# Optimization experiments

Measured on AMD Instinct MI355X. Metric: run time of the kernel, lower is better.

Reference implementation:

```python
import jax, jax.numpy as jnp
import numpy as np

H = 4096        # hidden_size
NH = 32         # heads
HD = H // NH    # head_dim = 128
EPS = 1e-5
MINUS_INF = -10000.0
B, S = 2, 1024


def setup_inputs() -> dict:
    key = jax.random.key(0)
    ks = jax.random.split(key, 7)
    x = jax.random.normal(ks[0], (B, S, H), jnp.float32)
    mask = jnp.zeros((B, 1, 1, S), jnp.float32)  # additive padding mask (0 = keep)
    norm_w = 1.0 + 0.02 * jax.random.normal(ks[1], (H,), jnp.float32)
    norm_b = 0.02 * jax.random.normal(ks[2], (H,), jnp.float32)
    qkv_w = 0.02 * jax.random.normal(ks[3], (H, 3 * H), jnp.float32)
    qkv_b = 0.02 * jax.random.normal(ks[4], (3 * H,), jnp.float32)
    attn_ow = 0.02 * jax.random.normal(ks[5], (H, H), jnp.float32)
    return {"x": x, "mask": mask, "norm_w": norm_w, "norm_b": norm_b,
            "qkv_w": qkv_w, "qkv_b": qkv_b, "attn_ow": attn_ow}


def reference(x, mask, norm_w, norm_b, qkv_w, qkv_b, attn_ow):
    b, s, h = x.shape
    # --- pre-attention layernorm (qkv_gemm fuses this in DeepSpeed) ---
    mu = jnp.mean(x, axis=-1, keepdims=True)
    var = jnp.mean(jnp.square(x - mu), axis=-1, keepdims=True)
    inp_norm = (x - mu) * jax.lax.rsqrt(var + EPS) * norm_w + norm_b
    # --- fused QKV GEMM + bias ---
    qkv = inp_norm @ qkv_w + qkv_b                      # [b, s, 3H]
    q, k, v = jnp.split(qkv, 3, axis=-1)
    q = q.reshape(b, s, NH, HD).transpose(0, 2, 1, 3)   # [b, nh, s, hd]
    k = k.reshape(b, s, NH, HD).transpose(0, 2, 1, 3)
    v = v.reshape(b, s, NH, HD).transpose(0, 2, 1, 3)
    # --- scaled dot-product with triangular (causal) mask + additive input mask ---
    norm_factor = 1.0 / jnp.sqrt(jnp.asarray(HD, x.dtype))
    scores = jnp.einsum('bhqd,bhkd->bhqk', q, k) * norm_factor  # [b, nh, s, s]
    causal = jnp.where(jnp.tril(jnp.ones((s, s), bool)), 0.0, MINUS_INF).astype(x.dtype)
    probs = jax.nn.softmax(scores + causal + mask, axis=-1)
    ctx = jnp.einsum('bhqk,bhkd->bhqd', probs, v)               # [b, nh, s, hd]
    ctx = ctx.transpose(0, 2, 1, 3).reshape(b, s, h)
    # --- output projection (vector_matmul, bias applied later in MLP residual-add) ---
    out = ctx @ attn_ow
    return out
```

## Files before the change

kernel.cpp:

```cpp
#include <hip/hip_runtime.h>
#include <stdint.h>


#define S_LEN 1024
#define HID   4096
#define NHEAD 32
#define HDIM  128

typedef __attribute__((ext_vector_type(8))) short bf16x8;
typedef __attribute__((ext_vector_type(4))) float f32x4;
typedef __attribute__((ext_vector_type(8))) unsigned short us8;

__device__ __forceinline__ unsigned short f2bf(float f) {
    union { float f; unsigned u; } v; v.f = f;
    unsigned r = v.u + 0x7fffu + ((v.u >> 16) & 1u);
    return (unsigned short)(r >> 16);
}

__device__ __forceinline__ void gld16(const unsigned short* g, unsigned short* l) {
    __builtin_amdgcn_global_load_lds(
        (const __attribute__((address_space(1))) void*)g,
        (__attribute__((address_space(3))) void*)l, 16, 0, 0);
}

__global__ __launch_bounds__(256) void ln_kernel(const float* __restrict__ x,
        const float* __restrict__ w, const float* __restrict__ bch,
        unsigned short* __restrict__ out) {
    const int row = blockIdx.x;
    const int t = threadIdx.x;
    const float* xr = x + (size_t)row * HID;
    float4 v[4];
    float sum = 0.f, sq = 0.f;
#pragma unroll
    for (int i = 0; i < 4; i++) {
        v[i] = ((const float4*)xr)[t + (i << 8)];
        sum += v[i].x + v[i].y + v[i].z + v[i].w;
        sq  += v[i].x*v[i].x + v[i].y*v[i].y + v[i].z*v[i].z + v[i].w*v[i].w;
    }
#pragma unroll
    for (int off = 32; off; off >>= 1) {
        sum += __shfl_down(sum, off);
        sq  += __shfl_down(sq, off);
    }
    __shared__ float ssum[4], ssq[4];
    if ((t & 63) == 0) { ssum[t >> 6] = sum; ssq[t >> 6] = sq; }
    __syncthreads();
    const float s_all = ssum[0] + ssum[1] + ssum[2] + ssum[3];
    const float q_all = ssq[0] + ssq[1] + ssq[2] + ssq[3];
    const float mean = s_all * (1.f / HID);
    const float var  = q_all * (1.f / HID) - mean * mean;
    const float rstd = rsqrtf(var + 1e-5f);
    unsigned short* orow = out + (size_t)row * HID;
#pragma unroll
    for (int i = 0; i < 4; i++) {
        float4 wv = ((const float4*)w)[t + (i << 8)];
        float4 bv = ((const float4*)bch)[t + (i << 8)];
        ushort4 o;
        o.x = f2bf((v[i].x - mean) * rstd * wv.x + bv.x);
        o.y = f2bf((v[i].y - mean) * rstd * wv.y + bv.y);
        o.z = f2bf((v[i].z - mean) * rstd * wv.z + bv.z);
        o.w = f2bf((v[i].w - mean) * rstd * wv.w + bv.w);
        ((ushort4*)orow)[t + (i << 8)] = o;
    }
}

__global__ __launch_bounds__(256) void transconv(const float* __restrict__ W,
        unsigned short* __restrict__ Wt, int K, int N) {
    __shared__ float tileT[128 * 65];
    const int n0 = blockIdx.x << 7, k0 = blockIdx.y << 6;
    const int t = threadIdx.x;
#pragma unroll
    for (int it = 0; it < 8; it++) {
        int idx = (it << 8) + t;
        int r = idx >> 5;
        int c4 = idx & 31;
        float4 v = *(const float4*)(W + (size_t)(k0 + r) * N + n0 + (c4 << 2));
        tileT[((c4 << 2) + 0) * 65 + r] = v.x;
        tileT[((c4 << 2) + 1) * 65 + r] = v.y;
        tileT[((c4 << 2) + 2) * 65 + r] = v.z;
        tileT[((c4 << 2) + 3) * 65 + r] = v.w;
    }
    __syncthreads();
#pragma unroll
    for (int it = 0; it < 4; it++) {
        int idx = (it << 8) + t;
        int n = idx >> 3;
        int k8 = idx & 7;
        const float* src = &tileT[n * 65 + (k8 << 3)];
        us8 o;
#pragma unroll
        for (int e = 0; e < 8; e++) o[e] = f2bf(src[e]);
        *(us8*)(Wt + (size_t)(n0 + n) * K + k0 + (k8 << 3)) = o;
    }
}

__global__ __launch_bounds__(256) void gemm_qkv(
        const unsigned short* __restrict__ A,
        const unsigned short* __restrict__ Bt,
        const float* __restrict__ bias,
        unsigned short* __restrict__ qb,
        unsigned short* __restrict__ kb,
        unsigned short* __restrict__ vt,
        int K) {
    __shared__ unsigned short a_lds[128 * 32];
    __shared__ unsigned short b_lds[128 * 32];
    const int t = threadIdx.x;
    const int wave = t >> 6, lane = t & 63, quad = lane >> 4, l16 = lane & 15;
    const int wm = (wave >> 1) << 6, wn = (wave & 1) << 6;
    const int bm = blockIdx.x, bn = blockIdx.y;
    const unsigned short* Ab = A  + (size_t)(bm << 7) * K;
    const unsigned short* Bb = Bt + (size_t)(bn << 7) * K;

    const f32x4 fz = {0.f, 0.f, 0.f, 0.f};
    f32x4 acc[4][4];
#pragma unroll
    for (int i = 0; i < 4; i++)
#pragma unroll
        for (int j = 0; j < 4; j++) acc[i][j] = fz;

    const int r0 = t >> 2;
    const int c_el = (t & 3) << 3;

    for (int k0 = 0; k0 < K; k0 += 32) {
#pragma unroll
        for (int issue = 0; issue < 2; issue++) {
            int row = r0 + (issue << 6);
            unsigned short* abase = a_lds + (((issue << 8) + (wave << 6)) << 3);
            unsigned short* bbase = b_lds + (((issue << 8) + (wave << 6)) << 3);
            gld16(Ab + (size_t)row * K + k0 + c_el, abase);
            gld16(Bb + (size_t)row * K + k0 + c_el, bbase);
        }
        __syncthreads();
        bf16x8 af[4], bfr[4];
        const bf16x8* av = (const bf16x8*)a_lds;
        const bf16x8* bv = (const bf16x8*)b_lds;
#pragma unroll
        for (int i = 0; i < 4; i++) af[i]  = av[((wm + (i << 4) + l16) << 2) + quad];
#pragma unroll
        for (int j = 0; j < 4; j++) bfr[j] = bv[((wn + (j << 4) + l16) << 2) + quad];
#pragma unroll
        for (int i = 0; i < 4; i++)
#pragma unroll
            for (int j = 0; j < 4; j++)
                acc[i][j] = __builtin_amdgcn_mfma_f32_16x16x32_bf16(af[i], bfr[j], acc[i][j], 0, 0, 0);
        __syncthreads();
    }

#pragma unroll
    for (int i = 0; i < 4; i++) {
#pragma unroll
        for (int j = 0; j < 4; j++) {
#pragma unroll
            for (int r = 0; r < 4; r++) {
                int m = (bm << 7) + wm + (i << 4) + (quad << 2) + r;
                int n = (bn << 7) + wn + (j << 4) + l16;
                float v = acc[i][j][r] + bias[n];
                unsigned short bvv = f2bf(v);
                int bb = m >> 10, s = m & 1023;
                int which = n >> 12;
                int h = n & 4095, head = h >> 7, hd = h & 127;
                size_t bh = (size_t)(bb << 5) + head;
                if (which == 0)      qb[(bh * S_LEN + s) * HDIM + hd] = bvv;
                else if (which == 1) kb[(bh * S_LEN + s) * HDIM + hd] = bvv;
                else                 vt[(bh * HDIM + hd) * S_LEN + s] = bvv;
            }
        }
    }
}

__global__ __launch_bounds__(256) void gemm_proj(
        const unsigned short* __restrict__ A,
        const unsigned short* __restrict__ Bt,
        float* __restrict__ outf,
        int K, int N) {
    __shared__ unsigned short a_lds[128 * 32];
    __shared__ unsigned short b_lds[128 * 32];
    const int t = threadIdx.x;
    const int wave = t >> 6, lane = t & 63, quad = lane >> 4, l16 = lane & 15;
    const int wm = (wave >> 1) << 6, wn = (wave & 1) << 6;
    const int bm = blockIdx.x, bn = blockIdx.y;
    const unsigned short* Ab = A  + (size_t)(bm << 7) * K;
    const unsigned short* Bb = Bt + (size_t)(bn << 7) * K;

    const f32x4 fz = {0.f, 0.f, 0.f, 0.f};
    f32x4 acc[4][4];
#pragma unroll
    for (int i = 0; i < 4; i++)
#pragma unroll
        for (int j = 0; j < 4; j++) acc[i][j] = fz;

    const int r0 = t >> 2;
    const int c_el = (t & 3) << 3;

    for (int k0 = 0; k0 < K; k0 += 32) {
#pragma unroll
        for (int issue = 0; issue < 2; issue++) {
            int row = r0 + (issue << 6);
            unsigned short* abase = a_lds + (((issue << 8) + (wave << 6)) << 3);
            unsigned short* bbase = b_lds + (((issue << 8) + (wave << 6)) << 3);
            gld16(Ab + (size_t)row * K + k0 + c_el, abase);
            gld16(Bb + (size_t)row * K + k0 + c_el, bbase);
        }
        __syncthreads();
        bf16x8 af[4], bfr[4];
        const bf16x8* av = (const bf16x8*)a_lds;
        const bf16x8* bv = (const bf16x8*)b_lds;
#pragma unroll
        for (int i = 0; i < 4; i++) af[i]  = av[((wm + (i << 4) + l16) << 2) + quad];
#pragma unroll
        for (int j = 0; j < 4; j++) bfr[j] = bv[((wn + (j << 4) + l16) << 2) + quad];
#pragma unroll
        for (int i = 0; i < 4; i++)
#pragma unroll
            for (int j = 0; j < 4; j++)
                acc[i][j] = __builtin_amdgcn_mfma_f32_16x16x32_bf16(af[i], bfr[j], acc[i][j], 0, 0, 0);
        __syncthreads();
    }

#pragma unroll
    for (int i = 0; i < 4; i++)
#pragma unroll
        for (int j = 0; j < 4; j++)
#pragma unroll
            for (int r = 0; r < 4; r++) {
                int m = (bm << 7) + wm + (i << 4) + (quad << 2) + r;
                int n = (bn << 7) + wn + (j << 4) + l16;
                outf[(size_t)m * N + n] = acc[i][j][r];
            }
}

__global__ __launch_bounds__(256) void attn_kernel(
        const unsigned short* __restrict__ qbuf,
        const unsigned short* __restrict__ kbuf,
        const unsigned short* __restrict__ vtbuf,
        const float* __restrict__ mask,
        unsigned short* __restrict__ ctx) {
    __shared__ unsigned short q_lds[64 * 128];
    __shared__ unsigned short k_lds[64 * 128];
    __shared__ unsigned short v_lds[128 * 64];
    __shared__ unsigned short p_lds[64 * 64];
    const int t = threadIdx.x;
    const int wave = t >> 6, lane = t & 63, quad = lane >> 4, l16 = lane & 15;
    const int bq = blockIdx.x, bh = blockIdx.y;
    const int q0 = bq << 6;
    const int b = bh >> 5;
    const unsigned short* Q  = qbuf  + (size_t)bh * S_LEN * HDIM;
    const unsigned short* Kp = kbuf  + (size_t)bh * S_LEN * HDIM;
    const unsigned short* Vp = vtbuf + (size_t)bh * HDIM * S_LEN;

    {
        int r = t >> 4, c = (t & 15) << 3;
#pragma unroll
        for (int it = 0; it < 4; it++)
            gld16(Q + (size_t)(q0 + r + (it << 4)) * HDIM + c,
                  q_lds + ((((it << 8) + (wave << 6))) << 3));
    }

    const f32x4 fz = {0.f, 0.f, 0.f, 0.f};
    f32x4 o[8];
#pragma unroll
    for (int n = 0; n < 8; n++) o[n] = fz;
    float l_i[4] = {0.f, 0.f, 0.f, 0.f};
    const float scale = 0.08838834764831845f;
    const float* mrow = mask + b * S_LEN;

    for (int kt = 0; kt <= bq; kt++) {
        const int k0 = kt << 6;
        {
            int rk = t >> 4, ck = (t & 15) << 3;
            int rv = t >> 3, cv = (t & 7) << 3;
#pragma unroll
            for (int it = 0; it < 4; it++) {
                gld16(Kp + (size_t)(k0 + rk + (it << 4)) * HDIM + ck,
                      k_lds + (((it << 8) + (wave << 6)) << 3));
                gld16(Vp + (size_t)(rv + (it << 5)) * S_LEN + k0 + cv,
                      v_lds + (((it << 8) + (wave << 6)) << 3));
            }
        }
        __syncthreads();

        f32x4 sacc[4];
#pragma unroll
        for (int j = 0; j < 4; j++) sacc[j] = fz;
        const bf16x8* qv = (const bf16x8*)q_lds;
        const bf16x8* kv = (const bf16x8*)k_lds;
#pragma unroll
        for (int kk = 0; kk < 4; kk++) {
            bf16x8 aq = qv[(((wave << 4) + l16) << 4) + (kk << 2) + quad];
#pragma unroll
            for (int j = 0; j < 4; j++) {
                bf16x8 bk = kv[((((j << 4) + l16)) << 4) + (kk << 2) + quad];
                sacc[j] = __builtin_amdgcn_mfma_f32_16x16x32_bf16(aq, bk, sacc[j], 0, 0, 0);
            }
        }

#pragma unroll
        for (int r = 0; r < 4; r++) {
            int qrow = q0 + (wave << 4) + (quad << 2) + r;
#pragma unroll
            for (int j = 0; j < 4; j++) {
                int key = k0 + (j << 4) + l16;
                float x = sacc[j][r] * scale + mrow[key];
                if (key > qrow) x -= 10000.0f;
                float p = __expf(x);
                l_i[r] += p;
                p_lds[((wave << 4) + (quad << 2) + r) * 64 + (j << 4) + l16] = f2bf(p);
            }
        }
        __syncthreads();

        const bf16x8* pvv = (const bf16x8*)p_lds;
        const bf16x8* vv = (const bf16x8*)v_lds;
#pragma unroll
        for (int ks = 0; ks < 2; ks++) {
            bf16x8 ap = pvv[(((wave << 4) + l16) << 3) + (ks << 2) + quad];
#pragma unroll
            for (int n = 0; n < 8; n++) {
                bf16x8 bvv = vv[((((n << 4) + l16)) << 3) + (ks << 2) + quad];
                o[n] = __builtin_amdgcn_mfma_f32_16x16x32_bf16(ap, bvv, o[n], 0, 0, 0);
            }
        }
        __syncthreads();
    }

#pragma unroll
    for (int r = 0; r < 4; r++) {
        float l = l_i[r];
#pragma unroll
        for (int off = 1; off < 16; off <<= 1) l += __shfl_xor(l, off);
        float inv = 1.0f / l;
        int qrow = q0 + (wave << 4) + (quad << 2) + r;
        size_t base = ((size_t)(b * S_LEN + qrow)) * HID + ((size_t)(bh & 31) << 7);
#pragma unroll
        for (int n = 0; n < 8; n++)
            ctx[base + (n << 4) + l16] = f2bf(o[n][r] * inv);
    }
}

extern "C" void kernel_launch(void* const* d_in, const int* in_sizes, int n_in,
                              void* d_out, int out_size, void* d_ws, size_t ws_size,
                              hipStream_t stream) {
    const float* x       = (const float*)d_in[0];
    const float* mask    = (const float*)d_in[1];
    const float* norm_w  = (const float*)d_in[2];
    const float* norm_b  = (const float*)d_in[3];
    const float* qkv_w   = (const float*)d_in[4];
    const float* qkv_b   = (const float*)d_in[5];
    const float* attn_ow = (const float*)d_in[6];
    float* out = (float*)d_out;

    char* ws = (char*)d_ws;
    size_t off = 0;
    auto alloc = [&](size_t bytes) {
        char* p = ws + off;
        off += (bytes + 255) & ~(size_t)255;
        return p;
    };
    unsigned short* inp_norm = (unsigned short*)alloc((size_t)2048 * HID * 2);
    unsigned short* qkv_wt   = (unsigned short*)alloc((size_t)3 * HID * HID * 2);
    unsigned short* ow_t     = (unsigned short*)alloc((size_t)HID * HID * 2);
    unsigned short* qb       = (unsigned short*)alloc((size_t)64 * S_LEN * HDIM * 2);
    unsigned short* kb       = (unsigned short*)alloc((size_t)64 * S_LEN * HDIM * 2);
    unsigned short* vt       = (unsigned short*)alloc((size_t)64 * S_LEN * HDIM * 2);
    unsigned short* ctx      = (unsigned short*)alloc((size_t)2048 * HID * 2);

    ln_kernel<<<2048, 256, 0, stream>>>(x, norm_w, norm_b, inp_norm);
    transconv<<<dim3(3 * HID / 128, HID / 64), 256, 0, stream>>>(qkv_w, qkv_wt, HID, 3 * HID);
    transconv<<<dim3(HID / 128, HID / 64), 256, 0, stream>>>(attn_ow, ow_t, HID, HID);
    gemm_qkv<<<dim3(16, 96), 256, 0, stream>>>(inp_norm, qkv_wt, qkv_b, qb, kb, vt, HID);
    attn_kernel<<<dim3(16, 64), 256, 0, stream>>>(qb, kb, vt, mask, ctx);
    gemm_proj<<<dim3(16, 32), 256, 0, stream>>>(ctx, ow_t, out, HID, HID);
}
```

Measured before the change: 878.8 us.

## Rewrite QKV and projection GEMMs with 8-wave triple-buffered pipelined core

Replaces the simple 128x128, 4-wave, single-buffered GEMMs with a 512-thread, 128x256 tile core. The core triple-buffers LDS with async global-to-LDS prefetch two tiles ahead, swizzles LDS to avoid bank conflicts, raises wave priority around MFMA bursts, and remaps block IDs for L2/XCD locality. The goal is to hide global-load latency and cut the per-iteration syncthreads stalls that dominate the old loop. It uses much more LDS (144KB per block with launch bounds of 2 blocks) and hardcodes K=4096.

```diff
diff --git a/kernel.cpp b/kernel.cpp
--- a/kernel.cpp
+++ b/kernel.cpp
@@ -94,22 +94,98 @@
     }
 }
 
-__global__ __launch_bounds__(256) void gemm_qkv(
+
+#define GEMM_PHASE(CB, KS, PFT, PFB, DO_VM)                                       \
+  {                                                                               \
+    bf16x8 af[4], bfv[4];                                                         \
+    _Pragma("unroll") for (int ii = 0; ii < 4; ii++) af[ii] = ldA(CB, KS, ii);    \
+    _Pragma("unroll") for (int jj = 0; jj < 4; jj++) bfv[jj] = ldB(CB, KS, jj);   \
+    stageA(PFT, KS, PFB);                                                         \
+    stageB(PFT, KS, PFB);                                                         \
+    __builtin_amdgcn_s_barrier();                                                 \
+    asm volatile("s_waitcnt lgkmcnt(0)" ::: "memory");                            \
+    __builtin_amdgcn_sched_barrier(0);                                            \
+    __builtin_amdgcn_s_setprio(1);                                                \
+    _Pragma("unroll") for (int ii = 0; ii < 4; ii++)                              \
+      _Pragma("unroll") for (int jj = 0; jj < 4; jj++)                            \
+        acc[ii][jj] = __builtin_amdgcn_mfma_f32_16x16x32_bf16(                    \
+            af[ii], bfv[jj], acc[ii][jj], 0, 0, 0);                               \
+    __builtin_amdgcn_s_setprio(0);                                                \
+    if (DO_VM) asm volatile("s_waitcnt vmcnt(6)" ::: "memory");                   \
+    __builtin_amdgcn_s_barrier();                                                 \
+  }
+
+#define GEMM_TILE(TT, CB)                                                         \
+  {                                                                               \
+    int pf_ = (TT) + 2; if (pf_ > 63) pf_ = 63;                                   \
+    GEMM_PHASE(CB, 0, pf_, ((CB) + 2) % 3, 0)                                     \
+    GEMM_PHASE(CB, 1, pf_, ((CB) + 2) % 3, 1)                                     \
+  }
+
+__device__ __forceinline__ void gemm_core_8w(
+        const unsigned short* __restrict__ GA,
+        const unsigned short* __restrict__ GB,
+        unsigned short* lds,
+        f32x4 acc[4][4]) {
+    const int t = threadIdx.x;
+    const int wave = t >> 6, lane = t & 63, quad = lane >> 4, l16 = lane & 15;
+    const int waveM = wave >> 2, waveN = wave & 3;
+    const int srow = lane >> 2;
+    const int scol = (((lane & 3) ^ ((lane >> 3) & 3)) << 3);
+
+    auto stageA = [&](int tau, int ks, int buf) {
+        const int row = (wave << 4) + srow;
+        gld16(GA + ((size_t)row << 12) + (tau << 6) + (ks << 5) + scol,
+              lds + buf * 24576 + (ks << 12) + (wave << 9));
+    };
+    auto stageB = [&](int tau, int ks, int buf) {
+#pragma unroll
+        for (int u = 0; u < 2; u++) {
+            const int ii = (wave << 1) + u;
+            const int row = (ii << 4) + srow;
+            gld16(GB + ((size_t)row << 12) + (tau << 6) + (ks << 5) + scol,
+                  lds + buf * 24576 + 8192 + (ks << 13) + (ii << 9));
+        }
+    };
+    auto ldA = [&](int buf, int ks, int ii) -> bf16x8 {
+        const int r = (waveM << 6) + (ii << 4) + l16;
+        return ((const bf16x8*)(lds + buf * 24576 + (ks << 12)))
+            [(r << 2) + (quad ^ ((r >> 1) & 3))];
+    };
+    auto ldB = [&](int buf, int ks, int jj) -> bf16x8 {
+        const int r = (waveN << 6) + (jj << 4) + l16;
+        return ((const bf16x8*)(lds + buf * 24576 + 8192 + (ks << 13)))
+            [(r << 2) + (quad ^ ((r >> 1) & 3))];
+    };
+
+    stageA(0, 0, 0); stageB(0, 0, 0); stageA(0, 1, 0); stageB(0, 1, 0);
+    stageA(1, 0, 1); stageB(1, 0, 1); stageA(1, 1, 1); stageB(1, 1, 1);
+    asm volatile("s_waitcnt vmcnt(6)" ::: "memory");
+    __builtin_amdgcn_s_barrier();
+
+    for (int tb = 0; tb < 63; tb += 3) {
+        GEMM_TILE(tb,     0)
+        GEMM_TILE(tb + 1, 1)
+        GEMM_TILE(tb + 2, 2)
+    }
+    GEMM_TILE(63, 0)
+    asm volatile("s_waitcnt vmcnt(0)" ::: "memory");
+}
+
+__global__ __launch_bounds__(512, 2) void gemm_qkv8(
         const unsigned short* __restrict__ A,
         const unsigned short* __restrict__ Bt,
         const float* __restrict__ bias,
         unsigned short* __restrict__ qb,
         unsigned short* __restrict__ kb,
-        unsigned short* __restrict__ vt,
-        int K) {
-    __shared__ unsigned short a_lds[128 * 32];
-    __shared__ unsigned short b_lds[128 * 32];
+        unsigned short* __restrict__ vt) {
+    __shared__ unsigned short lds[73728];
+    const int orig = blockIdx.x;
+    const int wg = ((orig & 7) * 96) + (orig >> 3);
+    const int bm = wg / 48, bn = wg - bm * 48;
     const int t = threadIdx.x;
     const int wave = t >> 6, lane = t & 63, quad = lane >> 4, l16 = lane & 15;
-    const int wm = (wave >> 1) << 6, wn = (wave & 1) << 6;
-    const int bm = blockIdx.x, bn = blockIdx.y;
-    const unsigned short* Ab = A  + (size_t)(bm << 7) * K;
-    const unsigned short* Bb = Bt + (size_t)(bn << 7) * K;
+    const int waveM = wave >> 2, waveN = wave & 3;
 
     const f32x4 fz = {0.f, 0.f, 0.f, 0.f};
     f32x4 acc[4][4];
@@ -118,46 +194,21 @@
 #pragma unroll
         for (int j = 0; j < 4; j++) acc[i][j] = fz;
 
-    const int r0 = t >> 2;
-    const int c_el = (t & 3) << 3;
-
-    for (int k0 = 0; k0 < K; k0 += 32) {
-#pragma unroll
-        for (int issue = 0; issue < 2; issue++) {
-            int row = r0 + (issue << 6);
-            unsigned short* abase = a_lds + (((issue << 8) + (wave << 6)) << 3);
-            unsigned short* bbase = b_lds + (((issue << 8) + (wave << 6)) << 3);
-            gld16(Ab + (size_t)row * K + k0 + c_el, abase);
-            gld16(Bb + (size_t)row * K + k0 + c_el, bbase);
-        }
-        __syncthreads();
-        bf16x8 af[4], bfr[4];
-        const bf16x8* av = (const bf16x8*)a_lds;
-        const bf16x8* bv = (const bf16x8*)b_lds;
-#pragma unroll
-        for (int i = 0; i < 4; i++) af[i]  = av[((wm + (i << 4) + l16) << 2) + quad];
-#pragma unroll
-        for (int j = 0; j < 4; j++) bfr[j] = bv[((wn + (j << 4) + l16) << 2) + quad];
-#pragma unroll
-        for (int i = 0; i < 4; i++)
-#pragma unroll
-            for (int j = 0; j < 4; j++)
-                acc[i][j] = __builtin_amdgcn_mfma_f32_16x16x32_bf16(af[i], bfr[j], acc[i][j], 0, 0, 0);
-        __syncthreads();
-    }
-
-#pragma unroll
-    for (int i = 0; i < 4; i++) {
-#pragma unroll
-        for (int j = 0; j < 4; j++) {
+    gemm_core_8w(A + ((size_t)bm << 19), Bt + ((size_t)bn << 20), lds, acc);
+
+    const int nbase = (bn << 8) + (waveN << 6);
+    const int which = nbase >> 12;
+#pragma unroll
+    for (int ii = 0; ii < 4; ii++) {
+#pragma unroll
+        for (int jj = 0; jj < 4; jj++) {
 #pragma unroll
             for (int r = 0; r < 4; r++) {
-                int m = (bm << 7) + wm + (i << 4) + (quad << 2) + r;
-                int n = (bn << 7) + wn + (j << 4) + l16;
-                float v = acc[i][j][r] + bias[n];
+                int m = (bm << 7) + (waveM << 6) + (ii << 4) + (quad << 2) + r;
+                int n = nbase + (jj << 4) + l16;
+                float v = acc[ii][jj][r] + bias[n];
                 unsigned short bvv = f2bf(v);
                 int bb = m >> 10, s = m & 1023;
-                int which = n >> 12;
                 int h = n & 4095, head = h >> 7, hd = h & 127;
                 size_t bh = (size_t)(bb << 5) + head;
                 if (which == 0)      qb[(bh * S_LEN + s) * HDIM + hd] = bvv;
@@ -168,19 +219,17 @@
     }
 }
 
-__global__ __launch_bounds__(256) void gemm_proj(
+__global__ __launch_bounds__(512, 2) void gemm_proj8(
         const unsigned short* __restrict__ A,
         const unsigned short* __restrict__ Bt,
-        float* __restrict__ outf,
-        int K, int N) {
-    __shared__ unsigned short a_lds[128 * 32];
-    __shared__ unsigned short b_lds[128 * 32];
+        float* __restrict__ outf) {
+    __shared__ unsigned short lds[73728];
+    const int orig = blockIdx.x;
+    const int wg = ((orig & 7) * 32) + (orig >> 3);
+    const int bm = wg >> 4, bn = wg & 15;
     const int t = threadIdx.x;
     const int wave = t >> 6, lane = t & 63, quad = lane >> 4, l16 = lane & 15;
-    const int wm = (wave >> 1) << 6, wn = (wave & 1) << 6;
-    const int bm = blockIdx.x, bn = blockIdx.y;
-    const unsigned short* Ab = A  + (size_t)(bm << 7) * K;
-    const unsigned short* Bb = Bt + (size_t)(bn << 7) * K;
+    const int waveM = wave >> 2, waveN = wave & 3;
 
     const f32x4 fz = {0.f, 0.f, 0.f, 0.f};
     f32x4 acc[4][4];
@@ -189,43 +238,17 @@
 #pragma unroll
         for (int j = 0; j < 4; j++) acc[i][j] = fz;
 
-    const int r0 = t >> 2;
-    const int c_el = (t & 3) << 3;
-
-    for (int k0 = 0; k0 < K; k0 += 32) {
-#pragma unroll
-        for (int issue = 0; issue < 2; issue++) {
-            int row = r0 + (issue << 6);
-            unsigned short* abase = a_lds + (((issue << 8) + (wave << 6)) << 3);
-            unsigned short* bbase = b_lds + (((issue << 8) + (wave << 6)) << 3);
-            gld16(Ab + (size_t)row * K + k0 + c_el, abase);
-            gld16(Bb + (size_t)row * K + k0 + c_el, bbase);
-        }
-        __syncthreads();
-        bf16x8 af[4], bfr[4];
-        const bf16x8* av = (const bf16x8*)a_lds;
-        const bf16x8* bv = (const bf16x8*)b_lds;
-#pragma unroll
-        for (int i = 0; i < 4; i++) af[i]  = av[((wm + (i << 4) + l16) << 2) + quad];
-#pragma unroll
-        for (int j = 0; j < 4; j++) bfr[j] = bv[((wn + (j << 4) + l16) << 2) + quad];
-#pragma unroll
-        for (int i = 0; i < 4; i++)
-#pragma unroll
-            for (int j = 0; j < 4; j++)
-                acc[i][j] = __builtin_amdgcn_mfma_f32_16x16x32_bf16(af[i], bfr[j], acc[i][j], 0, 0, 0);
-        __syncthreads();
-    }
-
-#pragma unroll
-    for (int i = 0; i < 4; i++)
-#pragma unroll
-        for (int j = 0; j < 4; j++)
+    gemm_core_8w(A + ((size_t)bm << 19), Bt + ((size_t)bn << 20), lds, acc);
+
+#pragma unroll
+    for (int ii = 0; ii < 4; ii++)
+#pragma unroll
+        for (int jj = 0; jj < 4; jj++)
 #pragma unroll
             for (int r = 0; r < 4; r++) {
-                int m = (bm << 7) + wm + (i << 4) + (quad << 2) + r;
-                int n = (bn << 7) + wn + (j << 4) + l16;
-                outf[(size_t)m * N + n] = acc[i][j][r];
+                int m = (bm << 7) + (waveM << 6) + (ii << 4) + (quad << 2) + r;
+                int n = (bn << 8) + (waveN << 6) + (jj << 4) + l16;
+                outf[((size_t)m << 12) + n] = acc[ii][jj][r];
             }
 }
 
@@ -367,7 +390,7 @@
     ln_kernel<<<2048, 256, 0, stream>>>(x, norm_w, norm_b, inp_norm);
     transconv<<<dim3(3 * HID / 128, HID / 64), 256, 0, stream>>>(qkv_w, qkv_wt, HID, 3 * HID);
     transconv<<<dim3(HID / 128, HID / 64), 256, 0, stream>>>(attn_ow, ow_t, HID, HID);
-    gemm_qkv<<<dim3(16, 96), 256, 0, stream>>>(inp_norm, qkv_wt, qkv_b, qb, kb, vt, HID);
+    gemm_qkv8<<<768, 512, 0, stream>>>(inp_norm, qkv_wt, qkv_b, qb, kb, vt);
     attn_kernel<<<dim3(16, 64), 256, 0, stream>>>(qb, kb, vt, mask, ctx);
-    gemm_proj<<<dim3(16, 32), 256, 0, stream>>>(ctx, ow_t, out, HID, HID);
-}
+    gemm_proj8<<<256, 512, 0, stream>>>(ctx, ow_t, out);
+}
```

Measured after the change: 839.0 us. 1.05x faster.
